# Kernel optimization log

Hardware: AMD Instinct MI355X
Metric: run time of the kernel (lower is better)

## Reference

```python
import jax, jax.numpy as jnp
import numpy as np

ITE = 20
LAM = 0.1
MU1 = 0.1
MU2 = 0.1
RHO = 1.05
SHAPE = (4, 31, 128, 128)  # N, C, H, W


def setup_inputs() -> dict:
    key = jax.random.key(0)
    k1, k2 = jax.random.split(key)
    Y = jax.random.normal(k1, SHAPE, dtype=jnp.float32)
    inW = jax.random.uniform(k2, SHAPE, dtype=jnp.float32)  # positive weights (W^2)
    return {"Y": Y, "inW": inW}


def _shrink(x, t):
    # soft-threshold: sign(x) * max(|x| - t, 0)
    return jnp.sign(x) * jnp.maximum(jnp.abs(x) - t, 0.0)


def _diff_h(x):
    # circular convolution with kernel [1, -1] along width
    return x - jnp.roll(x, 1, axis=-1)


def _diff_v(x):
    # circular convolution with kernel [[1], [-1]] along height
    return x - jnp.roll(x, 1, axis=-2)


def reference(Y, inW):
    H, W = Y.shape[-2], Y.shape[-1]
    # p2o: PSF placed at top-left of (H, W) canvas, then fft2
    dh = jnp.zeros((H, W), jnp.float32).at[0, 0].set(1.0).at[0, 1].set(-1.0)
    dv = jnp.zeros((H, W), jnp.float32).at[0, 0].set(1.0).at[1, 0].set(-1.0)
    FH = jnp.fft.fft2(dh)
    FV = jnp.fft.fft2(dv)
    demo = jnp.abs(FH) ** 2 + jnp.abs(FV) ** 2  # [H, W] real
    FHc = jnp.conj(FH)
    FVc = jnp.conj(FV)

    def tv_solver(A, B, C, mu1, mu2):
        # Fourier-domain solve of (mu1 I + mu2 D^T D) Z = mu1 A + mu2 D^T [B; C]
        num = mu1 * jnp.fft.fft2(A) + mu2 * (FHc * jnp.fft.fft2(B) + FVc * jnp.fft.fft2(C))
        return jnp.real(jnp.fft.ifft2(num / (mu1 + mu2 * demo)))

    zeros = jnp.zeros_like(Y)
    carry = (Y, Y, zeros, zeros, zeros, _diff_h(Y), _diff_v(Y),
             jnp.float32(MU1), jnp.float32(MU2))

    def body(c, _):
        Z, X, G1, G21, G22, DhZ, DvZ, mu1, mu2 = c
        Uh = _shrink(DhZ - G21 / mu2, LAM / mu2)
        Uv = _shrink(DvZ - G22 / mu2, LAM / mu2)
        Z = tv_solver(X + G1 / mu1, Uh + G21 / mu2, Uv + G22 / mu2, mu1, mu2)
        DhZ = _diff_h(Z)
        DvZ = _diff_v(Z)
        X = (inW * Y + mu1 * Z - G1) / (inW + mu1)
        G1 = G1 + mu1 * (X - Z)
        G21 = G21 + mu2 * (Uh - DhZ)
        G22 = G22 + mu2 * (Uv - DvZ)
        return (Z, X, G1, G21, G22, DhZ, DvZ, RHO * mu1, RHO * mu2), None

    (Z, *_), _ = jax.lax.scan(body, carry, None, length=ITE)
    return Z
```

## Files before the change

### kernel.cpp

```cpp
#include <hip/hip_runtime.h>


#define NPIX   16384
#define NSIDE  128
#define NIMG   124
#define NT     1024
#define PXT    16
#define N_ITE  20
#define LAM_F  0.1f
#define RHO_F  1.05f
#define PI_F   3.14159265358979323846f

#define SW(c) ((c) ^ ((c) >> 3))

__device__ __forceinline__ float2 cadd(float2 a, float2 b) {
    return make_float2(a.x + b.x, a.y + b.y);
}
__device__ __forceinline__ float2 csub(float2 a, float2 b) {
    return make_float2(a.x - b.x, a.y - b.y);
}
__device__ __forceinline__ float2 cmul(float2 a, float2 w) {
    return make_float2(fmaf(a.x, w.x, -(a.y * w.y)),
                       fmaf(a.x, w.y,  (a.y * w.x)));
}
__device__ __forceinline__ float2 cmulc(float2 a, float2 w) {
    return make_float2(fmaf(a.x, w.x,  (a.y * w.y)),
                       fmaf(a.y, w.x, -(a.x * w.y)));
}

#define RT2H 0.70710678118654752f

__device__ __forceinline__ void radix8_fwd(float2 z[8]) {
    float2 A0 = cadd(z[0], z[4]), A1 = cadd(z[1], z[5]);
    float2 A2 = cadd(z[2], z[6]), A3 = cadd(z[3], z[7]);
    float2 d0 = csub(z[0], z[4]), d1 = csub(z[1], z[5]);
    float2 d2 = csub(z[2], z[6]), d3 = csub(z[3], z[7]);
    float2 B0 = d0;
    float2 B1 = make_float2(RT2H*(d1.x + d1.y), RT2H*(d1.y - d1.x));
    float2 B2 = make_float2(d2.y, -d2.x);
    float2 B3 = make_float2(RT2H*(d3.y - d3.x), -RT2H*(d3.x + d3.y));
    float2 C0 = cadd(A0, A2), C2 = csub(A0, A2);
    float2 t13 = csub(A1, A3);
    float2 C1 = cadd(A1, A3);
    float2 C3 = make_float2(t13.y, -t13.x);
    float2 E0 = cadd(B0, B2), E2 = csub(B0, B2);
    float2 u13 = csub(B1, B3);
    float2 E1 = cadd(B1, B3);
    float2 E3 = make_float2(u13.y, -u13.x);
    z[0] = cadd(C0, C1);  z[1] = csub(C0, C1);
    z[2] = cadd(C2, C3);  z[3] = csub(C2, C3);
    z[4] = cadd(E0, E1);  z[5] = csub(E0, E1);
    z[6] = cadd(E2, E3);  z[7] = csub(E2, E3);
}

__device__ __forceinline__ void radix8_inv(float2 z[8]) {
    float2 a0 = cadd(z[0], z[1]), a1 = csub(z[0], z[1]);
    float2 a2 = cadd(z[2], z[3]), a3 = csub(z[2], z[3]);
    float2 a4 = cadd(z[4], z[5]), a5 = csub(z[4], z[5]);
    float2 a6 = cadd(z[6], z[7]), a7 = csub(z[6], z[7]);
    float2 b0 = cadd(a0, a2), b2 = csub(a0, a2);
    float2 t3 = make_float2(-a3.y, a3.x);
    float2 b1 = cadd(a1, t3), b3 = csub(a1, t3);
    float2 b4 = cadd(a4, a6), b6 = csub(a4, a6);
    float2 t7 = make_float2(-a7.y, a7.x);
    float2 b5 = cadd(a5, t7), b7 = csub(a5, t7);
    float2 p0 = b4;
    float2 p1 = make_float2(RT2H*(b5.x - b5.y), RT2H*(b5.x + b5.y));
    float2 p2 = make_float2(-b6.y, b6.x);
    float2 p3 = make_float2(-RT2H*(b7.x + b7.y), RT2H*(b7.x - b7.y));
    z[0] = cadd(b0, p0);  z[4] = csub(b0, p0);
    z[1] = cadd(b1, p1);  z[5] = csub(b1, p1);
    z[2] = cadd(b2, p2);  z[6] = csub(b2, p2);
    z[3] = cadd(b3, p3);  z[7] = csub(b3, p3);
}

__global__ __launch_bounds__(NT, 4) void hwtv_kernel(
    const float* __restrict__ Yg,
    const float* __restrict__ Wg,
    float* __restrict__ outg)
{
    extern __shared__ char smem[];
    float2* C  = (float2*)smem;
    float2* TW = (float2*)(smem + (size_t)NPIX * 8);
    float*  D1 = (float*)(smem + (size_t)NPIX * 8 + 64*8);

    const int tid = threadIdx.x;
    const size_t base  = (size_t)blockIdx.x * NPIX;
    const float* Y  = Yg + base;
    const float* Wt = Wg + base;
    float* out = outg + base;

    if (tid < 64) {
        float ang = -2.0f * PI_F * (float)tid / 128.0f;
        TW[tid] = make_float2(cosf(ang), sinf(ang));
    }
    if (tid < 128) {
        int br = (int)(__brev((unsigned)tid) >> 25);
        float s = sinf(PI_F * (float)br / 128.0f);
        D1[tid] = 4.0f * s * s;
    }

    float a[PXT], g1[PXT], bh[PXT], bv[PXT];
    #pragma unroll
    for (int k = 0; k < PXT; ++k) {
        int p = tid + k * NT;
        int col = p & (NSIDE - 1);
        int rowb = p & ~(NSIDE - 1);
        float y = Y[p];
        C[rowb + SW(col)] = make_float2(y, 0.0f);
        a[k]  = 0.1f * y;
        g1[k] = 0.0f;
        bh[k] = 0.0f;
        bv[k] = 0.0f;
    }
    __syncthreads();

    float mu1 = 0.1f, mu2 = 0.1f;

    for (int it = 0; it < N_ITE; ++it) {
        const float mu2p   = mu2 * (1.0f / RHO_F);
        const float inv_m2 = 1.0f / mu2;
        const float thr    = LAM_F * inv_m2;

        #pragma unroll 4
        for (int k = 0; k < PXT; ++k) {
            int p    = tid + k * NT;
            int col  = p & (NSIDE - 1);
            int rowb = p & ~(NSIDE - 1);
            int sc_  = SW(col);
            float z  = C[rowb + sc_].x;
            float zl = C[rowb + SW((col + NSIDE - 1) & (NSIDE - 1))].x;
            int pu   = (p + NPIX - NSIDE) & (NPIX - 1);
            float zu = C[(pu & ~(NSIDE - 1)) + sc_].x;
            float dhz = z - zl;
            float dvz = z - zu;
            float g21 = (it == 0) ? 0.0f : fmaf(-mu2p, dhz, bh[k]);
            float g22 = (it == 0) ? 0.0f : fmaf(-mu2p, dvz, bv[k]);
            float ah = dhz - g21 * inv_m2;
            float av = dvz - g22 * inv_m2;
            float uh = copysignf(fmaxf(fabsf(ah) - thr, 0.0f), ah);
            float uv = copysignf(fmaxf(fabsf(av) - thr, 0.0f), av);
            bh[k] = fmaf(mu2, uh, g21);
            bv[k] = fmaf(mu2, uv, g22);
        }
        __syncthreads();

        #pragma unroll 4
        for (int k = 0; k < PXT; ++k) {
            int p = tid + k * NT;
            int col = p & (NSIDE - 1);
            int rowb = p & ~(NSIDE - 1);
            C[rowb + SW(col)] = make_float2(bh[k], bv[k]);
        }
        __syncthreads();

        float numv[PXT];
        #pragma unroll 4
        for (int k = 0; k < PXT; ++k) {
            int p    = tid + k * NT;
            int col  = p & (NSIDE - 1);
            int rowb = p & ~(NSIDE - 1);
            int sc_  = SW(col);
            float bhr = C[rowb + SW((col + 1) & (NSIDE - 1))].x;
            int pd    = (p + NSIDE) & (NPIX - 1);
            float bvd = C[(pd & ~(NSIDE - 1)) + sc_].y;
            numv[k] = a[k] + (bh[k] - bhr) + (bv[k] - bvd);
        }
        __syncthreads();

        #pragma unroll 4
        for (int k = 0; k < PXT; ++k) {
            int p = tid + k * NT;
            int col = p & (NSIDE - 1);
            int rowb = p & ~(NSIDE - 1);
            C[rowb + SW(col)] = make_float2(numv[k], 0.0f);
        }
        __syncthreads();

        #define FWD_ROW_PASS(S, L2)                                          \
        {                                                                    \
            _Pragma("unroll 2")                                              \
            for (int q = 0; q < 4; ++q) {                                    \
                int m   = tid + q * NT;                                      \
                int rb  = (m >> 5) << 7;                                     \
                int b   = m & 31;                                            \
                int j   = b & ((L2) - 1);                                    \
                int i0  = ((b & ~((L2) - 1)) << 2) | j;                      \
                int e0 = rb + SW(i0);                                        \
                int e1 = rb + SW(i0 + (L2));                                 \
                int e2 = rb + SW(i0 + 2*(L2));                               \
                int e3 = rb + SW(i0 + 3*(L2));                               \
                float2 w1 = TW[j << (S)];                                    \
                float2 w2 = cmul(w1, w1);                                    \
                float2 x0 = C[e0], x1 = C[e1];                               \
                float2 x2 = C[e2], x3 = C[e3];                               \
                float2 t02p = cadd(x0, x2);                                  \
                float2 t13p = cadd(x1, x3);                                  \
                float2 t02m = cmul(csub(x0, x2), w1);                        \
                float2 uu   = cmul(csub(x1, x3), w1);                        \
                float2 t13m = make_float2(uu.y, -uu.x);          \
                C[e0] = cadd(t02p, t13p);                                    \
                C[e1] = cmul(csub(t02p, t13p), w2);                          \
                C[e2] = cadd(t02m, t13m);                                    \
                C[e3] = cmul(csub(t02m, t13m), w2);                          \
            }                                                                \
            __syncthreads();                                                 \
        }
        FWD_ROW_PASS(0, 32)
        FWD_ROW_PASS(2, 8)
        {
            #pragma unroll 2
            for (int q = 0; q < 2; ++q) {
                int m  = tid + q * NT;
                int rb = (m >> 4) << 7;
                int cb = (m & 15) << 3;
                float2 z[8];
                #pragma unroll
                for (int i = 0; i < 8; ++i) z[i] = C[rb + SW(cb + i)];
                radix8_fwd(z);
                #pragma unroll
                for (int i = 0; i < 8; ++i) C[rb + SW(cb + i)] = z[i];
            }
            __syncthreads();
        }

        #define FWD_COL_PASS(S, L2)                                          \
        {                                                                    \
            _Pragma("unroll 2")                                              \
            for (int q = 0; q < 4; ++q) {                                    \
                int m  = tid + q * NT;                                       \
                int c  = m & 127;                                            \
                int b  = m >> 7;                                             \
                int j  = b & ((L2) - 1);                                     \
                int i0 = ((b & ~((L2) - 1)) << 2) | j;                       \
                int p0 = (i0 << 7) + SW(c);                                  \
                const int ST = (L2) << 7;                                    \
                float2 w1 = TW[j << (S)];                                    \
                float2 w2 = cmul(w1, w1);                                    \
                float2 x0 = C[p0], x1 = C[p0 + ST];                          \
                float2 x2 = C[p0 + 2*ST], x3 = C[p0 + 3*ST];                 \
                float2 t02p = cadd(x0, x2);                                  \
                float2 t13p = cadd(x1, x3);                                  \
                float2 t02m = cmul(csub(x0, x2), w1);                        \
                float2 uu   = cmul(csub(x1, x3), w1);                        \
                float2 t13m = make_float2(uu.y, -uu.x);                      \
                C[p0]        = cadd(t02p, t13p);                             \
                C[p0 +   ST] = cmul(csub(t02p, t13p), w2);                   \
                C[p0 + 2*ST] = cadd(t02m, t13m);                             \
                C[p0 + 3*ST] = cmul(csub(t02m, t13m), w2);                   \
            }                                                                \
            __syncthreads();                                                 \
        }
        FWD_COL_PASS(0, 32)
        FWD_COL_PASS(2, 8)

        {
            const float sc = 1.0f / (float)NPIX;
            #pragma unroll 2
            for (int q = 0; q < 2; ++q) {
                int m   = tid + q * NT;
                int col = m & 127;
                int g   = m >> 7;
                int r0  = g << 3;
                int p0  = (r0 << 7) + SW(col);
                float2 z[8];
                #pragma unroll
                for (int i = 0; i < 8; ++i) z[i] = C[p0 + (i << 7)];
                radix8_fwd(z);
                float d1c = D1[col];
                #pragma unroll
                for (int i = 0; i < 8; ++i) {
                    float f = sc / fmaf(mu2, D1[r0 + i] + d1c, mu1);
                    z[i].x *= f; z[i].y *= f;
                }
                radix8_inv(z);
                #pragma unroll
                for (int i = 0; i < 8; ++i) C[p0 + (i << 7)] = z[i];
            }
            __syncthreads();
        }

        #define INV_COL_PASS(SB, M)                                          \
        {                                                                    \
            _Pragma("unroll 2")                                              \
            for (int q = 0; q < 4; ++q) {                                    \
                int m  = tid + q * NT;                                       \
                int c  = m & 127;                                            \
                int b  = m >> 7;                                             \
                int j  = b & ((M) - 1);                                      \
                int i0 = ((b & ~((M) - 1)) << 2) | j;                        \
                int p0 = (i0 << 7) + SW(c);                                  \
                const int ST = (M) << 7;                                     \
                float2 wb = TW[j << (SB)];                                   \
                float2 wa = cmul(wb, wb);                                    \
                float2 x0 = C[p0], x1 = C[p0 + ST];                          \
                float2 x2 = C[p0 + 2*ST], x3 = C[p0 + 3*ST];                 \
                float2 pp1 = cmulc(x1, wa);                                  \
                float2 a0 = cadd(x0, pp1), a1 = csub(x0, pp1);               \
                float2 pp2 = cmulc(x3, wa);                                  \
                float2 a2 = cadd(x2, pp2), a3 = csub(x2, pp2);               \
                float2 q0 = cmulc(a2, wb);                                   \
                float2 y0 = cadd(a0, q0), y2 = csub(a0, q0);                 \
                float2 uu = cmulc(a3, wb);                                   \
                float2 q1 = make_float2(-uu.y, uu.x);            \
                float2 y1 = cadd(a1, q1), y3 = csub(a1, q1);                 \
                C[p0]        = y0;                                           \
                C[p0 +   ST] = y1;                                           \
                C[p0 + 2*ST] = y2;                                           \
                C[p0 + 3*ST] = y3;                                           \
            }                                                                \
            __syncthreads();                                                 \
        }
        INV_COL_PASS(2, 8)
        INV_COL_PASS(0, 32)

        {
            #pragma unroll 2
            for (int q = 0; q < 2; ++q) {
                int m  = tid + q * NT;
                int rb = (m >> 4) << 7;
                int cb = (m & 15) << 3;
                float2 z[8];
                #pragma unroll
                for (int i = 0; i < 8; ++i) z[i] = C[rb + SW(cb + i)];
                radix8_inv(z);
                #pragma unroll
                for (int i = 0; i < 8; ++i) C[rb + SW(cb + i)] = z[i];
            }
            __syncthreads();
        }
        #define INV_ROW_PASS(SB, M)                                          \
        {                                                                    \
            _Pragma("unroll 2")                                              \
            for (int q = 0; q < 4; ++q) {                                    \
                int m   = tid + q * NT;                                      \
                int rb  = (m >> 5) << 7;                                     \
                int b   = m & 31;                                            \
                int j   = b & ((M) - 1);                                     \
                int i0  = ((b & ~((M) - 1)) << 2) | j;                       \
                int e0 = rb + SW(i0);                                        \
                int e1 = rb + SW(i0 + (M));                                  \
                int e2 = rb + SW(i0 + 2*(M));                                \
                int e3 = rb + SW(i0 + 3*(M));                                \
                float2 wb = TW[j << (SB)];                                   \
                float2 wa = cmul(wb, wb);                                    \
                float2 x0 = C[e0], x1 = C[e1];                               \
                float2 x2 = C[e2], x3 = C[e3];                               \
                float2 pp1 = cmulc(x1, wa);                                  \
                float2 a0 = cadd(x0, pp1), a1 = csub(x0, pp1);               \
                float2 pp2 = cmulc(x3, wa);                                  \
                float2 a2 = cadd(x2, pp2), a3 = csub(x2, pp2);               \
                float2 q0 = cmulc(a2, wb);                                   \
                float2 y0 = cadd(a0, q0), y2 = csub(a0, q0);                 \
                float2 uu = cmulc(a3, wb);                                   \
                float2 q1 = make_float2(-uu.y, uu.x);                        \
                float2 y1 = cadd(a1, q1), y3 = csub(a1, q1);                 \
                C[e0] = y0;                                                  \
                C[e1] = y1;                                                  \
                C[e2] = y2;                                                  \
                C[e3] = y3;                                                  \
            }                                                                \
            __syncthreads();                                                 \
        }
        INV_ROW_PASS(2, 8)
        INV_ROW_PASS(0, 32)

        const float mu1n = mu1 * RHO_F;
        #pragma unroll 4
        for (int k = 0; k < PXT; ++k) {
            int p = tid + k * NT;
            int col = p & (NSIDE - 1);
            int rowb = p & ~(NSIDE - 1);
            float z  = C[rowb + SW(col)].x;
            float y  = Y[p];
            float w  = Wt[p];
            float x  = fmaf(w, y, fmaf(mu1, z, -g1[k])) *
                       __builtin_amdgcn_rcpf(w + mu1);
            g1[k] = fmaf(mu1, x - z, g1[k]);
            a[k]  = fmaf(mu1n, x, g1[k]);
            if (it == N_ITE - 1) out[p] = z;
        }

        mu1 *= RHO_F;
        mu2 *= RHO_F;
    }
}

extern "C" void kernel_launch(void* const* d_in, const int* in_sizes, int n_in,
                              void* d_out, int out_size, void* d_ws, size_t ws_size,
                              hipStream_t stream) {
    (void)in_sizes; (void)n_in; (void)out_size; (void)d_ws; (void)ws_size;
    const float* Y   = (const float*)d_in[0];
    const float* inW = (const float*)d_in[1];
    float* out = (float*)d_out;

    const size_t smem_bytes = (size_t)NPIX * 8 + 64 * 8 + 128 * 4;
    hipFuncSetAttribute((const void*)hwtv_kernel,
                        hipFuncAttributeMaxDynamicSharedMemorySize,
                        (int)smem_bytes);
    hipLaunchKernelGGL(hwtv_kernel, dim3(NIMG), dim3(NT), smem_bytes, stream,
                       Y, inW, out);
}
```

Before: 660.8 us.

## Replace row-pass block barriers with wave-local waits and fuse X update into shrink

The radix-8 row stages are remapped so each wavefront owns whole rows across every row FFT pass. That lets the barriers between row passes become a wave-local LDS wait (s_waitcnt lgkmcnt(0)) instead of block-wide __syncthreads. The X/G1 update, which used to be a separate pass at the end of each iteration, is moved into the next iteration's shrinkage pass using the previous mu1, and the output is written once after the loop. Scratch stores now write single floats instead of float2 pairs. The risk is correctness: the code relies on row ownership staying strictly within one wavefront and on the wave executing in lockstep.

```diff
diff --git a/kernel.cpp b/kernel.cpp
--- a/kernel.cpp
+++ b/kernel.cpp
@@ -12,6 +12,8 @@
 #define PI_F   3.14159265358979323846f
 
 #define SW(c) ((c) ^ ((c) >> 3))
+
+#define WSYNC() asm volatile("s_waitcnt lgkmcnt(0)" ::: "memory")
 
 __device__ __forceinline__ float2 cadd(float2 a, float2 b) {
     return make_float2(a.x + b.x, a.y + b.y);
@@ -100,7 +102,7 @@
         D1[tid] = 4.0f * s * s;
     }
 
-    float a[PXT], g1[PXT], bh[PXT], bv[PXT];
+    float g1[PXT], bh[PXT], bv[PXT];
     #pragma unroll
     for (int k = 0; k < PXT; ++k) {
         int p = tid + k * NT;
@@ -108,7 +110,6 @@
         int rowb = p & ~(NSIDE - 1);
         float y = Y[p];
         C[rowb + SW(col)] = make_float2(y, 0.0f);
-        a[k]  = 0.1f * y;
         g1[k] = 0.0f;
         bh[k] = 0.0f;
         bv[k] = 0.0f;
@@ -118,10 +119,12 @@
     float mu1 = 0.1f, mu2 = 0.1f;
 
     for (int it = 0; it < N_ITE; ++it) {
+        const float mu1p   = mu1 * (1.0f / RHO_F);
         const float mu2p   = mu2 * (1.0f / RHO_F);
         const float inv_m2 = 1.0f / mu2;
         const float thr    = LAM_F * inv_m2;
 
+        float a[PXT];
         #pragma unroll 4
         for (int k = 0; k < PXT; ++k) {
             int p    = tid + k * NT;
@@ -132,6 +135,16 @@
             float zl = C[rowb + SW((col + NSIDE - 1) & (NSIDE - 1))].x;
             int pu   = (p + NPIX - NSIDE) & (NPIX - 1);
             float zu = C[(pu & ~(NSIDE - 1)) + sc_].x;
+            float y  = Y[p];
+            float w  = Wt[p];
+            if (it == 0) {
+                a[k] = 0.1f * y;
+            } else {
+                float x = fmaf(w, y, fmaf(mu1p, z, -g1[k])) *
+                          __builtin_amdgcn_rcpf(w + mu1p);
+                g1[k] = fmaf(mu1p, x - z, g1[k]);
+                a[k]  = fmaf(mu1, x, g1[k]);
+            }
             float dhz = z - zl;
             float dvz = z - zu;
             float g21 = (it == 0) ? 0.0f : fmaf(-mu2p, dhz, bh[k]);
@@ -142,6 +155,7 @@
             float uv = copysignf(fmaxf(fabsf(av) - thr, 0.0f), av);
             bh[k] = fmaf(mu2, uh, g21);
             bv[k] = fmaf(mu2, uv, g22);
+            ((float*)&C[rowb + sc_])[1] = bh[k];
         }
         __syncthreads();
 
@@ -150,7 +164,7 @@
             int p = tid + k * NT;
             int col = p & (NSIDE - 1);
             int rowb = p & ~(NSIDE - 1);
-            C[rowb + SW(col)] = make_float2(bh[k], bv[k]);
+            ((float*)&C[rowb + SW(col)])[0] = bv[k];
         }
         __syncthreads();
 
@@ -161,9 +175,9 @@
             int col  = p & (NSIDE - 1);
             int rowb = p & ~(NSIDE - 1);
             int sc_  = SW(col);
-            float bhr = C[rowb + SW((col + 1) & (NSIDE - 1))].x;
+            float bhr = ((float*)&C[rowb + SW((col + 1) & (NSIDE - 1))])[1];
             int pd    = (p + NSIDE) & (NPIX - 1);
-            float bvd = C[(pd & ~(NSIDE - 1)) + sc_].y;
+            float bvd = ((float*)&C[(pd & ~(NSIDE - 1)) + sc_])[0];
             numv[k] = a[k] + (bh[k] - bhr) + (bv[k] - bvd);
         }
         __syncthreads();
@@ -204,25 +218,27 @@
                 C[e2] = cadd(t02m, t13m);                                    \
                 C[e3] = cmul(csub(t02m, t13m), w2);                          \
             }                                                                \
-            __syncthreads();                                                 \
         }
         FWD_ROW_PASS(0, 32)
+        WSYNC();
         FWD_ROW_PASS(2, 8)
+        WSYNC();
         {
+            const int wv = tid >> 6, l = tid & 63;
             #pragma unroll 2
             for (int q = 0; q < 2; ++q) {
-                int m  = tid + q * NT;
-                int rb = (m >> 4) << 7;
-                int cb = (m & 15) << 3;
-                float2 z[8];
-                #pragma unroll
-                for (int i = 0; i < 8; ++i) z[i] = C[rb + SW(cb + i)];
-                radix8_fwd(z);
-                #pragma unroll
-                for (int i = 0; i < 8; ++i) C[rb + SW(cb + i)] = z[i];
+                int rowsel = (q << 2) | (l >> 4);
+                int rb = ((2*wv + (rowsel & 1) + ((rowsel >> 1) << 5)) << 7);
+                int cb = (l & 15) << 3;
+                float2 zz[8];
+                #pragma unroll
+                for (int i = 0; i < 8; ++i) zz[i] = C[rb + SW(cb + i)];
+                radix8_fwd(zz);
+                #pragma unroll
+                for (int i = 0; i < 8; ++i) C[rb + SW(cb + i)] = zz[i];
             }
-            __syncthreads();
-        }
+        }
+        __syncthreads();
 
         #define FWD_COL_PASS(S, L2)                                          \
         {                                                                    \
@@ -249,10 +265,11 @@
                 C[p0 + 2*ST] = cadd(t02m, t13m);                             \
                 C[p0 + 3*ST] = cmul(csub(t02m, t13m), w2);                   \
             }                                                                \
-            __syncthreads();                                                 \
         }
         FWD_COL_PASS(0, 32)
+        __syncthreads();
         FWD_COL_PASS(2, 8)
+        __syncthreads();
 
         {
             const float sc = 1.0f / (float)NPIX;
@@ -263,22 +280,22 @@
                 int g   = m >> 7;
                 int r0  = g << 3;
                 int p0  = (r0 << 7) + SW(col);
-                float2 z[8];
-                #pragma unroll
-                for (int i = 0; i < 8; ++i) z[i] = C[p0 + (i << 7)];
-                radix8_fwd(z);
+                float2 zz[8];
+                #pragma unroll
+                for (int i = 0; i < 8; ++i) zz[i] = C[p0 + (i << 7)];
+                radix8_fwd(zz);
                 float d1c = D1[col];
                 #pragma unroll
                 for (int i = 0; i < 8; ++i) {
                     float f = sc / fmaf(mu2, D1[r0 + i] + d1c, mu1);
-                    z[i].x *= f; z[i].y *= f;
+                    zz[i].x *= f; zz[i].y *= f;
                 }
-                radix8_inv(z);
-                #pragma unroll
-                for (int i = 0; i < 8; ++i) C[p0 + (i << 7)] = z[i];
+                radix8_inv(zz);
+                #pragma unroll
+                for (int i = 0; i < 8; ++i) C[p0 + (i << 7)] = zz[i];
             }
-            __syncthreads();
-        }
+        }
+        __syncthreads();
 
         #define INV_COL_PASS(SB, M)                                          \
         {                                                                    \
@@ -309,26 +326,28 @@
                 C[p0 + 2*ST] = y2;                                           \
                 C[p0 + 3*ST] = y3;                                           \
             }                                                                \
-            __syncthreads();                                                 \
         }
         INV_COL_PASS(2, 8)
+        __syncthreads();
         INV_COL_PASS(0, 32)
+        __syncthreads();
 
         {
+            const int wv = tid >> 6, l = tid & 63;
             #pragma unroll 2
             for (int q = 0; q < 2; ++q) {
-                int m  = tid + q * NT;
-                int rb = (m >> 4) << 7;
-                int cb = (m & 15) << 3;
-                float2 z[8];
-                #pragma unroll
-                for (int i = 0; i < 8; ++i) z[i] = C[rb + SW(cb + i)];
-                radix8_inv(z);
-                #pragma unroll
-                for (int i = 0; i < 8; ++i) C[rb + SW(cb + i)] = z[i];
+                int rowsel = (q << 2) | (l >> 4);
+                int rb = ((2*wv + (rowsel & 1) + ((rowsel >> 1) << 5)) << 7);
+                int cb = (l & 15) << 3;
+                float2 zz[8];
+                #pragma unroll
+                for (int i = 0; i < 8; ++i) zz[i] = C[rb + SW(cb + i)];
+                radix8_inv(zz);
+                #pragma unroll
+                for (int i = 0; i < 8; ++i) C[rb + SW(cb + i)] = zz[i];
             }
-            __syncthreads();
-        }
+        }
+        WSYNC();
         #define INV_ROW_PASS(SB, M)                                          \
         {                                                                    \
             _Pragma("unroll 2")                                              \
@@ -360,29 +379,22 @@
                 C[e2] = y2;                                                  \
                 C[e3] = y3;                                                  \
             }                                                                \
-            __syncthreads();                                                 \
         }
         INV_ROW_PASS(2, 8)
+        WSYNC();
         INV_ROW_PASS(0, 32)
-
-        const float mu1n = mu1 * RHO_F;
-        #pragma unroll 4
-        for (int k = 0; k < PXT; ++k) {
-            int p = tid + k * NT;
-            int col = p & (NSIDE - 1);
-            int rowb = p & ~(NSIDE - 1);
-            float z  = C[rowb + SW(col)].x;
-            float y  = Y[p];
-            float w  = Wt[p];
-            float x  = fmaf(w, y, fmaf(mu1, z, -g1[k])) *
-                       __builtin_amdgcn_rcpf(w + mu1);
-            g1[k] = fmaf(mu1, x - z, g1[k]);
-            a[k]  = fmaf(mu1n, x, g1[k]);
-            if (it == N_ITE - 1) out[p] = z;
-        }
+        __syncthreads();
 
         mu1 *= RHO_F;
         mu2 *= RHO_F;
+    }
+
+    #pragma unroll 4
+    for (int k = 0; k < PXT; ++k) {
+        int p = tid + k * NT;
+        int col = p & (NSIDE - 1);
+        int rowb = p & ~(NSIDE - 1);
+        out[p] = C[rowb + SW(col)].x;
     }
 }
 
```

Result: slower. 865.6 us (+31.0%).
